# Optimization experiments

Hardware: AMD Instinct MI355X
Metric: run time of the kernel (lower is better)

Reference implementation:

```python
import jax, jax.numpy as jnp
import numpy as np

B, T, D = 4, 2048, 1024

def setup_inputs() -> dict:
    key = jax.random.key(0)
    kx, kq, kk, kv = jax.random.split(key, 4)
    scale = 1.0 / np.sqrt(D)
    return {
        "x": jax.random.normal(kx, (B, T, D), dtype=jnp.float32),
        "Wq": jax.random.normal(kq, (D, D), dtype=jnp.float32) * scale,
        "Wk": jax.random.normal(kk, (D, D), dtype=jnp.float32) * scale,
        "Wv": jax.random.normal(kv, (D, D), dtype=jnp.float32) * scale,
    }

def reference(x, Wq, Wk, Wv):
    # torch Linear: y = x @ W.T (no bias, qkv_bias=False)
    q = jnp.einsum("btd,od->bto", x, Wq)
    k = jnp.einsum("btd,od->bto", x, Wk)
    v = jnp.einsum("btd,od->bto", x, Wv)
    scores = jnp.einsum("bqd,bkd->bqk", q, k)
    # NOTE: source uses non-in-place masked_fill whose result is discarded,
    # so NO causal mask is actually applied. Faithfully reproduced here.
    inv_sqrt_d = 1.0 / np.sqrt(k.shape[-1]).astype(np.float32)
    weights = jax.nn.softmax(scores * inv_sqrt_d, axis=-1)
    # dropout p=0.0 -> identity
    return jnp.einsum("bqk,bkd->bqd", weights, v)
```

## Files before the change

### kernel.cpp

```cpp
#include <hip/hip_runtime.h>
#include <hip/hip_bf16.h>
#include <hip/hip_fp16.h>
#include <type_traits>

typedef _Float16 f16;
typedef __attribute__((ext_vector_type(8))) _Float16 f16x8;
typedef __attribute__((ext_vector_type(4))) float floatx4;

#define B_ 4
#define T_ 2048
#define D_ 1024

#define XB_OFF   0ul
#define WB_OFF   16777216ul
#define QKV_OFF  23068672ul
#define S_OFF    73400320ul
#define VT_OFF   0ul

#define ASYNC16(gp, lp) \
    __builtin_amdgcn_global_load_lds((const __attribute__((address_space(1))) unsigned int*)(gp), \
                                     (__attribute__((address_space(3))) unsigned int*)(lp), 16, 0, 0)

__global__ __launch_bounds__(256) void cast_all(
    const float* __restrict__ x, const float* __restrict__ wq,
    const float* __restrict__ wk, const float* __restrict__ wv,
    f16* __restrict__ xb, f16* __restrict__ wb)
{
    long i = (long)blockIdx.x * 256 + threadIdx.x;
    const float4* src; f16* dst;
    if (i < 2097152L)            { src = (const float4*)x;  dst = xb; }
    else if (i < 2359296L)       { i -= 2097152L; src = (const float4*)wq; dst = wb; }
    else if (i < 2621440L)       { i -= 2359296L; src = (const float4*)wk; dst = wb + 1048576; }
    else                         { i -= 2621440L; src = (const float4*)wv; dst = wb + 2097152; }
    float4 v = src[i];
    union { f16 h[4]; uint2 u; } o;
    o.h[0] = (f16)v.x; o.h[1] = (f16)v.y; o.h[2] = (f16)v.z; o.h[3] = (f16)v.w;
    ((uint2*)dst)[i] = o.u;
}

template <typename CT, int BN, int WN>
__global__ __launch_bounds__(256, 2) void gemm_nt(
    const f16* __restrict__ A, int lda, long sA,
    const f16* __restrict__ B, int ldb, long sB,
    CT* __restrict__ C, int ldc, long sC,
    int K, float alpha)
{
    __shared__ f16 As[2][128 * 32];
    __shared__ f16 Bs[2][BN * 32];

    const int tid = threadIdx.x;
    const int m0 = blockIdx.y * 128;
    const int n0 = blockIdx.x * BN;
    const int bz = blockIdx.z;
    A += (long)bz * sA;
    B += (long)bz * sB;
    C += (long)bz * sC;

    const int w  = tid >> 6;
    const int l  = tid & 63;
    const int wm = (w >> 1) * 64;
    const int wn = (w & 1) * WN;
    const int lr = l & 15;
    const int kg = l >> 4;
    const int kx = kg ^ ((lr >> 1) & 3);

    constexpr int NI = WN / 16;
    floatx4 acc[4][NI] = {};

    const int srow = tid >> 2;
    const int gsl  = (tid & 3) ^ ((tid >> 3) & 3);
    const long ldaL = lda, ldbL = ldb;
    const f16* Aptr = A + (long)(m0 + srow) * ldaL + gsl * 8;
    const f16* Bptr = B + (long)(n0 + srow) * ldbL + gsl * 8;

    auto stage = [&](int b, int kk) {
        #pragma unroll
        for (int rh = 0; rh < 2; rh++)
            ASYNC16(Aptr + kk + rh * 64 * ldaL, &As[b][rh * 2048 + w * 512]);
        #pragma unroll
        for (int rh = 0; rh < BN / 64; rh++)
            ASYNC16(Bptr + kk + rh * 64 * ldbL, &Bs[b][rh * 2048 + w * 512]);
    };

    stage(0, 0);
    __syncthreads();

    for (int k0 = 0; k0 < K; k0 += 32) {
        const int cur = (k0 >> 5) & 1;
        if (k0 + 32 < K) stage(cur ^ 1, k0 + 32);

        f16x8 af[4], bf[NI];
        #pragma unroll
        for (int mi = 0; mi < 4; mi++)
            af[mi] = *(const f16x8*)&As[cur][(wm + mi * 16 + lr) * 32 + kx * 8];
        #pragma unroll
        for (int ni = 0; ni < NI; ni++)
            bf[ni] = *(const f16x8*)&Bs[cur][(wn + ni * 16 + lr) * 32 + kx * 8];
        #pragma unroll
        for (int mi = 0; mi < 4; mi++)
            #pragma unroll
            for (int ni = 0; ni < NI; ni++)
                acc[mi][ni] = __builtin_amdgcn_mfma_f32_16x16x32_f16(af[mi], bf[ni], acc[mi][ni], 0, 0, 0);

        __syncthreads();
    }

    #pragma unroll
    for (int mi = 0; mi < 4; mi++) {
        #pragma unroll
        for (int ni = 0; ni < NI; ni++) {
            #pragma unroll
            for (int r = 0; r < 4; r++) {
                int row = m0 + wm + mi * 16 + kg * 4 + r;
                int col = n0 + wn + ni * 16 + lr;
                float v = acc[mi][ni][r] * alpha;
                if constexpr (std::is_same<CT, float>::value)
                    C[(long)row * ldc + col] = v;
                else
                    C[(long)row * ldc + col] = (f16)v;
            }
        }
    }
}

__global__ __launch_bounds__(256) void transpose_v(const f16* __restrict__ qkv, f16* __restrict__ vt)
{
    __shared__ f16 tile[32][33];
    int b  = blockIdx.z;
    int j0 = blockIdx.x * 32;
    int d0 = blockIdx.y * 32;
    int tx = threadIdx.x & 31;
    int ty = threadIdx.x >> 5;
    #pragma unroll
    for (int i = 0; i < 4; i++) {
        int j = j0 + ty + i * 8;
        tile[ty + i * 8][tx] = qkv[((long)b * T_ + j) * 3072 + 2048 + d0 + tx];
    }
    __syncthreads();
    #pragma unroll
    for (int i = 0; i < 4; i++) {
        int d = d0 + ty + i * 8;
        vt[((long)b * D_ + d) * T_ + j0 + tx] = tile[tx][ty + i * 8];
    }
}

__global__ __launch_bounds__(256) void softmax_rows(f16* __restrict__ S)
{
    long row = (long)blockIdx.x * 4 + (threadIdx.x >> 6);
    int l = threadIdx.x & 63;
    uint4* p4 = (uint4*)(S + row * 2048);
    union U { uint4 u; f16 h[8]; } d[4];
    float v[32];
    float mx = -1e30f;
    #pragma unroll
    for (int i = 0; i < 4; i++) {
        d[i].u = p4[i * 64 + l];
        #pragma unroll
        for (int j = 0; j < 8; j++) { v[i * 8 + j] = (float)d[i].h[j]; mx = fmaxf(mx, v[i * 8 + j]); }
    }
    #pragma unroll
    for (int off = 32; off; off >>= 1) mx = fmaxf(mx, __shfl_xor(mx, off, 64));
    float s = 0.f;
    #pragma unroll
    for (int i = 0; i < 32; i++) { v[i] = __expf(v[i] - mx); s += v[i]; }
    #pragma unroll
    for (int off = 32; off; off >>= 1) s += __shfl_xor(s, off, 64);
    float inv = 1.f / s;
    #pragma unroll
    for (int i = 0; i < 4; i++) {
        #pragma unroll
        for (int j = 0; j < 8; j++) d[i].h[j] = (f16)(v[i * 8 + j] * inv);
        p4[i * 64 + l] = d[i].u;
    }
}

extern "C" void kernel_launch(void* const* d_in, const int* in_sizes, int n_in,
                              void* d_out, int out_size, void* d_ws, size_t ws_size,
                              hipStream_t stream)
{
    const float* x  = (const float*)d_in[0];
    const float* wq = (const float*)d_in[1];
    const float* wk = (const float*)d_in[2];
    const float* wv = (const float*)d_in[3];
    float* out = (float*)d_out;
    char* ws = (char*)d_ws;
    f16* xb  = (f16*)(ws + XB_OFF);
    f16* wb  = (f16*)(ws + WB_OFF);
    f16* qkv = (f16*)(ws + QKV_OFF);
    f16* s   = (f16*)(ws + S_OFF);
    f16* vt  = (f16*)(ws + VT_OFF);

    cast_all<<<11264, 256, 0, stream>>>(x, wq, wk, wv, xb, wb);

    gemm_nt<f16, 256, 128><<<dim3(12, 64, 1), 256, 0, stream>>>(
        xb, 1024, 0L, wb, 1024, 0L, qkv, 3072, 0L, 1024, 1.0f);

    transpose_v<<<dim3(64, 32, 4), 256, 0, stream>>>(qkv, vt);

    gemm_nt<f16, 256, 128><<<dim3(8, 16, 4), 256, 0, stream>>>(
        qkv,        3072, (long)T_ * 3072,
        qkv + 1024, 3072, (long)T_ * 3072,
        s,          2048, (long)T_ * 2048, 1024, 0.03125f);

    softmax_rows<<<2048, 256, 0, stream>>>(s);

    gemm_nt<float, 128, 64><<<dim3(8, 16, 4), 256, 0, stream>>>(
        s,  2048, (long)T_ * 2048,
        vt, 2048, (long)D_ * 2048,
        out, 1024, (long)T_ * 1024, 2048, 1.0f);
}
```

Baseline: 279.7 us.

## Triple-buffer GEMM LDS staging with vmcnt waits and single barrier per step

Changes the NT GEMM main loop from double buffering with two syncthreads per iteration to a three-stage ring of LDS buffers. Two tiles are prefetched ahead, and explicit s_waitcnt vmcnt lets only the oldest tile's async loads complete before a single barrier. This is meant to hide global-to-LDS latency better and cut synchronisation stalls. In exchange it uses more LDS per block, which may reduce occupancy. The hand-chosen vmcnt counts must match the number of outstanding async loads, and the one-barrier ring relies on that ordering to avoid overwriting a buffer that is still being read.

```diff
diff --git a/kernel.cpp b/kernel.cpp
--- a/kernel.cpp
+++ b/kernel.cpp
@@ -20,6 +20,13 @@
 #define ASYNC16(gp, lp) \
     __builtin_amdgcn_global_load_lds((const __attribute__((address_space(1))) unsigned int*)(gp), \
                                      (__attribute__((address_space(3))) unsigned int*)(lp), 16, 0, 0)
+
+template<int N> __device__ __forceinline__ void vmwait() {
+    if constexpr (N == 0)      asm volatile("s_waitcnt vmcnt(0)" ::: "memory");
+    else if constexpr (N == 4) asm volatile("s_waitcnt vmcnt(4)" ::: "memory");
+    else if constexpr (N == 6) asm volatile("s_waitcnt vmcnt(6)" ::: "memory");
+    else static_assert(N == 0, "unsupported vmcnt literal");
+}
 
 __global__ __launch_bounds__(256) void cast_all(
     const float* __restrict__ x, const float* __restrict__ wq,
@@ -45,8 +52,9 @@
     CT* __restrict__ C, int ldc, long sC,
     int K, float alpha)
 {
-    __shared__ f16 As[2][128 * 32];
-    __shared__ f16 Bs[2][BN * 32];
+    __shared__ f16 As[3][128 * 32];
+    __shared__ f16 Bs[3][BN * 32];
+    constexpr int L = 2 + BN / 64;
 
     const int tid = threadIdx.x;
     const int m0 = blockIdx.y * 128;
@@ -73,36 +81,44 @@
     const f16* Aptr = A + (long)(m0 + srow) * ldaL + gsl * 8;
     const f16* Bptr = B + (long)(n0 + srow) * ldbL + gsl * 8;
 
-    auto stage = [&](int b, int kk) {
+    auto stage = [&](f16* Ad, f16* Bd, int kk) {
         #pragma unroll
         for (int rh = 0; rh < 2; rh++)
-            ASYNC16(Aptr + kk + rh * 64 * ldaL, &As[b][rh * 2048 + w * 512]);
+            ASYNC16(Aptr + kk + rh * 64 * ldaL, Ad + rh * 2048 + w * 512);
         #pragma unroll
         for (int rh = 0; rh < BN / 64; rh++)
-            ASYNC16(Bptr + kk + rh * 64 * ldbL, &Bs[b][rh * 2048 + w * 512]);
+            ASYNC16(Bptr + kk + rh * 64 * ldbL, Bd + rh * 2048 + w * 512);
     };
 
-    stage(0, 0);
-    __syncthreads();
-
-    for (int k0 = 0; k0 < K; k0 += 32) {
-        const int cur = (k0 >> 5) & 1;
-        if (k0 + 32 < K) stage(cur ^ 1, k0 + 32);
+    f16 *a0 = As[0], *a1 = As[1], *a2 = As[2];
+    f16 *b0 = Bs[0], *b1 = Bs[1], *b2 = Bs[2];
+
+    const int NT = K >> 5;
+    stage(a0, b0, 0);
+    stage(a1, b1, 32);
+
+    for (int t = 0; t < NT; ++t) {
+        if (t < NT - 1) vmwait<L>(); else vmwait<0>();
+        __builtin_amdgcn_s_barrier();
+        __builtin_amdgcn_sched_barrier(0);
+
+        if (t + 2 < NT) stage(a2, b2, (t + 2) << 5);
 
         f16x8 af[4], bf[NI];
         #pragma unroll
         for (int mi = 0; mi < 4; mi++)
-            af[mi] = *(const f16x8*)&As[cur][(wm + mi * 16 + lr) * 32 + kx * 8];
+            af[mi] = *(const f16x8*)&a0[(wm + mi * 16 + lr) * 32 + kx * 8];
         #pragma unroll
         for (int ni = 0; ni < NI; ni++)
-            bf[ni] = *(const f16x8*)&Bs[cur][(wn + ni * 16 + lr) * 32 + kx * 8];
+            bf[ni] = *(const f16x8*)&b0[(wn + ni * 16 + lr) * 32 + kx * 8];
         #pragma unroll
         for (int mi = 0; mi < 4; mi++)
             #pragma unroll
             for (int ni = 0; ni < NI; ni++)
                 acc[mi][ni] = __builtin_amdgcn_mfma_f32_16x16x32_f16(af[mi], bf[ni], acc[mi][ni], 0, 0, 0);
 
-        __syncthreads();
+        f16* ta = a0; a0 = a1; a1 = a2; a2 = ta;
+        f16* tb = b0; b0 = b1; b1 = b2; b2 = tb;
     }
 
     #pragma unroll
```

After: 279.3 us. Within noise of the previous version (-0.1%).
